# Kernel optimization log

Hardware: AMD Instinct MI355X
Metric: run time of the kernel (lower is better)

## Reference

```python
import jax, jax.numpy as jnp
import numpy as np

HEADS = 8
RANK = 4

def _lora(x, w_down, w_up, palette, in_dim, out_dim):
    # w_down: [RANK*in_dim, 15], w_up: [RANK*out_dim, 15], palette: [1, 15]
    down = (palette @ w_down.T).reshape(RANK, in_dim)   # [r, in]
    up = (palette @ w_up.T).reshape(out_dim, RANK)      # [out, r]
    return (x @ down.T) @ up.T                          # [..., out]


def setup_inputs() -> dict:
    key = jax.random.key(0)
    ks = jax.random.split(key, 16)
    B, S, D = 2, 2048, 1280
    def n(k, shape, std=0.02):
        return (jax.random.normal(k, shape, dtype=jnp.float32) * std).astype(jnp.float32)
    return {
        'hidden_states': jax.random.normal(ks[0], (B, S, D), dtype=jnp.float32),
        'color_palette': jax.random.uniform(ks[1], (1, 15), dtype=jnp.float32),
        'Wq': n(ks[2], (D, D)), 'Wk': n(ks[3], (D, D)),
        'Wv': n(ks[4], (D, D)), 'Wo': n(ks[5], (D, D)),
        'bo': jnp.zeros((D,), dtype=jnp.float32),
        'q_down': n(ks[6], (RANK * D, 15), 0.25), 'q_up': n(ks[7], (RANK * D, 15)),
        'k_down': n(ks[8], (RANK * D, 15), 0.25), 'k_up': n(ks[9], (RANK * D, 15)),
        'v_down': n(ks[10], (RANK * D, 15), 0.25), 'v_up': n(ks[11], (RANK * D, 15)),
        'o_down': n(ks[12], (RANK * D, 15), 0.25), 'o_up': n(ks[13], (RANK * D, 15)),
    }


def reference(hidden_states, color_palette, Wq, Wk, Wv, Wo, bo,
              q_down, q_up, k_down, k_up, v_down, v_up, o_down, o_up):
    B, S, D = hidden_states.shape
    H = HEADS
    hd = D // H
    scale = 1.0  # LoRA scale
    x = hidden_states
    # LoRA-augmented projections (self-attention: encoder_hidden_states = x)
    q = x @ Wq.T + scale * _lora(x, q_down, q_up, color_palette, D, D)
    k = x @ Wk.T + scale * _lora(x, k_down, k_up, color_palette, D, D)
    v = x @ Wv.T + scale * _lora(x, v_down, v_up, color_palette, D, D)
    # split heads: [B, S, D] -> [B, H, S, hd]
    q = q.reshape(B, S, H, hd).transpose(0, 2, 1, 3)
    k = k.reshape(B, S, H, hd).transpose(0, 2, 1, 3)
    v = v.reshape(B, S, H, hd).transpose(0, 2, 1, 3)
    attn_scale = 1.0 / jnp.sqrt(jnp.asarray(hd, dtype=q.dtype))
    scores = jnp.einsum('bhqd,bhkd->bhqk', q, k) * attn_scale
    probs = jax.nn.softmax(scores, axis=-1)
    out = jnp.einsum('bhqk,bhkd->bhqd', probs, v)
    out = out.transpose(0, 2, 1, 3).reshape(B, S, D)
    out = out @ Wo.T + bo + scale * _lora(out, o_down, o_up, color_palette, D, D)
    return out
```

## Files before the change

kernel.cpp:

```cpp
#include <hip/hip_runtime.h>

typedef unsigned short u16;
typedef unsigned int u32;
typedef __attribute__((ext_vector_type(4))) float floatx4;
typedef __attribute__((ext_vector_type(16))) float floatx16;
typedef __attribute__((ext_vector_type(8))) __bf16 bf16x8;
typedef __attribute__((ext_vector_type(2))) unsigned int u32x2;
typedef __attribute__((ext_vector_type(4))) unsigned int u32x4;

#define MFMA_BF16(a, b, c) __builtin_amdgcn_mfma_f32_16x16x32_bf16((a), (b), (c), 0, 0, 0)
#define MFMA32(a, b, c) __builtin_amdgcn_mfma_f32_32x32x16_bf16((a), (b), (c), 0, 0, 0)

typedef const __attribute__((address_space(1))) void* gas_ptr;
typedef __attribute__((address_space(3))) void* las_ptr;

__device__ __forceinline__ void gll16(const void* g, void* l) {
  __builtin_amdgcn_global_load_lds((gas_ptr)g, (las_ptr)l, 16, 0, 0);
}

__device__ __forceinline__ u16 f2bf(float x) {
  u32 u = __builtin_bit_cast(u32, x);
  u = (u + 0x7fffu + ((u >> 16) & 1u)) >> 16;
  return (u16)u;
}

__device__ __forceinline__ u32 cvtpk(float lo, float hi) {
  u32 r;
  asm("v_cvt_pk_bf16_f32 %0, %1, %2" : "=v"(r) : "v"(lo), "v"(hi));
  return r;
}

template <int WN>
__device__ __forceinline__ void vwait() {
  if constexpr (WN == 6) asm volatile("s_waitcnt vmcnt(6)" ::: "memory");
  else if constexpr (WN == 4) asm volatile("s_waitcnt vmcnt(4)" ::: "memory");
}

__global__ void prep_downup(const float* __restrict__ pal,
                            const float* __restrict__ qd, const float* __restrict__ qu,
                            const float* __restrict__ kd, const float* __restrict__ ku,
                            const float* __restrict__ vd, const float* __restrict__ vu,
                            const float* __restrict__ od, const float* __restrict__ ou,
                            float* __restrict__ down_f, float* __restrict__ up_f) {
  int tid = blockIdx.x * blockDim.x + threadIdx.x;
  int w = tid / 10240;
  int rem = tid - w * 10240;
  const float* dsrc = (w == 0) ? qd : (w == 1) ? kd : (w == 2) ? vd : od;
  const float* usrc = (w == 0) ? qu : (w == 1) ? ku : (w == 2) ? vu : ou;
  bool isdown = rem < 5120;
  int row = isdown ? rem : rem - 5120;
  const float* src = (isdown ? dsrc : usrc) + row * 15;
  float s = 0.f;
#pragma unroll
  for (int p = 0; p < 15; ++p) s += pal[p] * src[p];
  if (isdown) down_f[w * 5120 + row] = s;
  else        up_f[w * 5120 + row] = s;
}

__global__ void build_weff(const float* __restrict__ Wq, const float* __restrict__ Wk,
                           const float* __restrict__ Wv, const float* __restrict__ Wo,
                           const float* __restrict__ down_f, const float* __restrict__ up_f,
                           u16* __restrict__ weff_qkv, u16* __restrict__ weff_o) {
  int tid = blockIdx.x * blockDim.x + threadIdx.x;
  int w = tid / 1638400;
  int rem = tid - w * 1638400;
  int n = rem / 1280;
  int k = rem - n * 1280;
  const float* W = (w == 0) ? Wq : (w == 1) ? Wk : (w == 2) ? Wv : Wo;
  const float* up = up_f + w * 5120 + n * 4;
  const float* dn = down_f + w * 5120 + k;
  float v = W[rem] + up[0] * dn[0] + up[1] * dn[1280] + up[2] * dn[2560] + up[3] * dn[3840];
  u16 hv = f2bf(v);
  if (w < 3) weff_qkv[w * 1638400 + rem] = hv;
  else       weff_o[rem] = hv;
}

__global__ void cvt_x(const float4* __restrict__ x, ushort4* __restrict__ xb) {
  int i = blockIdx.x * blockDim.x + threadIdx.x;
  float4 v = x[i];
  ushort4 o;
  o.x = f2bf(v.x); o.y = f2bf(v.y); o.z = f2bf(v.z); o.w = f2bf(v.w);
  xb[i] = o;
}

__global__ __launch_bounds__(512) void gemm256_qkv(const u16* __restrict__ A, const u16* __restrict__ Bm,
                                                   u16* __restrict__ qb, u16* __restrict__ kb,
                                                   u16* __restrict__ vbuf, int K) {
  __shared__ __align__(16) u16 lA[2][16384];
  __shared__ __align__(16) u16 lB[2][16384];
  const int t = threadIdx.x;
  const int lane = t & 63;
  const int l15 = lane & 15, quad = lane >> 4;
  const int wid = t >> 6;
  const int wm = wid >> 2;
  const int wn = wid & 3;
  const int bm = blockIdx.x * 256;
  const int bn = blockIdx.y * 256;
  floatx4 acc[8][4] = {};

  const int r0 = t >> 3, pos = t & 7;
  const long sof0 = (long)r0 * K + ((pos + r0) & 7) * 8;
  const long sof1 = (long)(r0 + 64) * K + ((pos + r0 + 64) & 7) * 8;

  int afo[4][2], bfo[2][2];
#pragma unroll
  for (int ch = 0; ch < 2; ++ch) {
    int kc8 = ch * 4 + quad;
#pragma unroll
    for (int mi = 0; mi < 4; ++mi) {
      int ra = wm * 128 + mi * 16 + l15;
      afo[mi][ch] = ra * 64 + ((kc8 - ra) & 7) * 8;
    }
#pragma unroll
    for (int ni = 0; ni < 2; ++ni) {
      int rb = wn * 64 + ni * 16 + l15;
      bfo[ni][ch] = rb * 64 + ((kc8 - rb) & 7) * 8;
    }
  }

  const u16* Ab = A + (long)bm * K;
  const u16* Bb = Bm + (long)bn * K;

#define PHASE(CB, Q, SB, SMAT, SH, ST, WN)                                           \
  {                                                                                   \
    const u16* gsrc = (SMAT) ? Bb : Ab;                                               \
    u16* ld0 = ((SMAT) ? &lB[SB][0] : &lA[SB][0]) + ((SH) * 1024 + t) * 8;            \
    gll16(gsrc + sof0 + (long)(SH) * 128 * K + (long)(ST) * 64, ld0);                 \
    gll16(gsrc + sof1 + (long)(SH) * 128 * K + (long)(ST) * 64, ld0 + 4096);          \
    vwait<WN>();                                                                      \
    __builtin_amdgcn_s_barrier();                                                     \
    __builtin_amdgcn_sched_barrier(0);                                                \
    constexpr int mh = (Q) >> 1, nh = (Q) & 1;                                        \
    bf16x8 af[4][2], bfr[2][2];                                                       \
    _Pragma("unroll") for (int ch = 0; ch < 2; ++ch) {                                \
      _Pragma("unroll") for (int mi = 0; mi < 4; ++mi)                                \
        af[mi][ch] = *(const bf16x8*)(&lA[CB][0] + afo[mi][ch] + mh * 4096);          \
      _Pragma("unroll") for (int ni = 0; ni < 2; ++ni)                                \
        bfr[ni][ch] = *(const bf16x8*)(&lB[CB][0] + bfo[ni][ch] + nh * 2048);         \
    }                                                                                 \
    asm volatile("s_waitcnt lgkmcnt(0)" ::: "memory");                                \
    __builtin_amdgcn_sched_barrier(0);                                                \
    __builtin_amdgcn_s_setprio(1);                                                    \
    _Pragma("unroll") for (int ch = 0; ch < 2; ++ch)                                  \
      _Pragma("unroll") for (int mi = 0; mi < 4; ++mi)                                \
        _Pragma("unroll") for (int ni = 0; ni < 2; ++ni)                              \
          acc[mh * 4 + mi][nh * 2 + ni] =                                             \
              MFMA_BF16(af[mi][ch], bfr[ni][ch], acc[mh * 4 + mi][nh * 2 + ni]);      \
    __builtin_amdgcn_s_setprio(0);                                                    \
  }

  gll16(Ab + sof0, &lA[0][t * 8]);
  gll16(Ab + sof1, &lA[0][t * 8 + 4096]);
  gll16(Bb + sof0, &lB[0][t * 8]);
  gll16(Bb + sof1, &lB[0][t * 8 + 4096]);
  gll16(Ab + sof0 + 128L * K, &lA[0][(1024 + t) * 8]);
  gll16(Ab + sof1 + 128L * K, &lA[0][(1024 + t) * 8 + 4096]);
  gll16(Bb + sof0 + 128L * K, &lB[0][(1024 + t) * 8]);
  gll16(Bb + sof1 + 128L * K, &lB[0][(1024 + t) * 8 + 4096]);

  const int niter = K >> 7;
  for (int i = 0; i < niter; ++i) {
    const int t1 = 2 * i + 1, t2 = 2 * i + 2;
    PHASE(0, 0, 1, 0, 0, t1, 6);
    PHASE(0, 1, 1, 1, 0, t1, 4);
    PHASE(0, 2, 1, 0, 1, t1, 0);
    PHASE(0, 3, 1, 1, 1, t1, 0);
    PHASE(1, 0, 0, 0, 0, t2, 6);
    PHASE(1, 1, 0, 1, 0, t2, 4);
    PHASE(1, 2, 0, 0, 1, t2, 0);
    PHASE(1, 3, 0, 1, 1, t2, 0);
  }
#undef PHASE
  asm volatile("s_waitcnt vmcnt(0)" ::: "memory");

#pragma unroll
  for (int mi8 = 0; mi8 < 8; ++mi8) {
#pragma unroll
    for (int ni4 = 0; ni4 < 4; ++ni4) {
#pragma unroll
      for (int r = 0; r < 4; ++r) {
        int m = bm + wm * 128 + (mi8 >> 2) * 64 + (mi8 & 3) * 16 + quad * 4 + r;
        int n = bn + wn * 64 + (ni4 >> 1) * 32 + (ni4 & 1) * 16 + l15;
        u16 hv = f2bf(acc[mi8][ni4][r]);
        if (n < 1280) {
          qb[(long)m * 1280 + n] = hv;
        } else if (n < 2560) {
          kb[(long)m * 1280 + (n - 1280)] = hv;
        } else {
          vbuf[(long)m * 1280 + (n - 2560)] = hv;
        }
      }
    }
  }
}

__global__ __launch_bounds__(256) void vtrans(const u16* __restrict__ vbuf,
                                              u16* __restrict__ vtb) {
  __shared__ u16 tile[64 * 65];
  const int t = threadIdx.x;
  const int sb = blockIdx.x * 64, nb = blockIdx.y * 64, b = blockIdx.z;
  const u16* src = vbuf + ((long)(b * 2048 + sb)) * 1280 + nb;
#pragma unroll
  for (int it = 0; it < 16; ++it) {
    int idx = t + it * 256;
    int s = idx >> 6, n = idx & 63;
    tile[s * 65 + n] = src[(long)s * 1280 + n];
  }
  __syncthreads();
  u16* dst = vtb + ((long)(b * 1280 + nb)) * 2048 + sb;
#pragma unroll
  for (int it = 0; it < 16; ++it) {
    int idx = t + it * 256;
    int n = idx >> 6, s = idx & 63;
    dst[(long)n * 2048 + s] = tile[s * 65 + n];
  }
}

__global__ __launch_bounds__(256) void gemm128_o(const u16* __restrict__ A, const u16* __restrict__ Bm,
                                                 float* __restrict__ outf,
                                                 const float* __restrict__ bias, int K) {
  __shared__ __align__(16) u16 lA[128 * 64];
  __shared__ __align__(16) u16 lB[128 * 64];
  const int t = threadIdx.x;
  const int lane = t & 63;
  const int l15 = lane & 15, quad = lane >> 4;
  const int wid = t >> 6;
  const int wm = (wid >> 1) * 64;
  const int wn = (wid & 1) * 64;
  const int bm = blockIdx.x * 128;
  const int bn = blockIdx.y * 128;
  floatx4 acc[4][4] = {};

  int soff[4];
#pragma unroll
  for (int i = 0; i < 4; ++i) {
    int c = t + i * 256;
    int row = c >> 3, pos = c & 7;
    soff[i] = row * K + ((pos + row) & 7) * 8;
  }
  int afo[4][2], bfo[4][2];
#pragma unroll
  for (int i = 0; i < 4; ++i) {
#pragma unroll
    for (int ch = 0; ch < 2; ++ch) {
      int ra = wm + i * 16 + l15;
      int rb = wn + i * 16 + l15;
      int kc8 = ch * 4 + quad;
      afo[i][ch] = ra * 64 + ((kc8 - ra) & 7) * 8;
      bfo[i][ch] = rb * 64 + ((kc8 - rb) & 7) * 8;
    }
  }

  const u16* Ab = A + (long)bm * K;
  const u16* Bb = Bm + (long)bn * K;
  const int nkt = K >> 6;

  for (int kt = 0; kt < nkt; ++kt) {
    __syncthreads();
    const int k0 = kt * 64;
#pragma unroll
    for (int i = 0; i < 4; ++i) gll16(Ab + (long)soff[i] + k0, lA + (t + i * 256) * 8);
#pragma unroll
    for (int i = 0; i < 4; ++i) gll16(Bb + (long)soff[i] + k0, lB + (t + i * 256) * 8);
    __syncthreads();
#pragma unroll
    for (int ch = 0; ch < 2; ++ch) {
      bf16x8 af[4], bfr[4];
#pragma unroll
      for (int i = 0; i < 4; ++i) af[i] = *(const bf16x8*)(lA + afo[i][ch]);
#pragma unroll
      for (int i = 0; i < 4; ++i) bfr[i] = *(const bf16x8*)(lB + bfo[i][ch]);
#pragma unroll
      for (int i = 0; i < 4; ++i)
#pragma unroll
        for (int j = 0; j < 4; ++j)
          acc[i][j] = MFMA_BF16(af[i], bfr[j], acc[i][j]);
    }
  }

#pragma unroll
  for (int i = 0; i < 4; ++i) {
#pragma unroll
    for (int j = 0; j < 4; ++j) {
#pragma unroll
      for (int r = 0; r < 4; ++r) {
        int m = bm + wm + i * 16 + quad * 4 + r;
        int n = bn + wn + j * 16 + l15;
        outf[(long)m * 1280 + n] = acc[i][j][r] + bias[n];
      }
    }
  }
}

__global__ __launch_bounds__(512) void flash_attn(const u16* __restrict__ qb,
                                                  const u16* __restrict__ kb,
                                                  const u16* __restrict__ vtb,
                                                  u16* __restrict__ attn) {
  const int D = 1280, HD = 160;
  __shared__ __align__(16) u16 kv_lds[2][20480];
  const int t = threadIdx.x, lane = t & 63, wid = t >> 6;
  const int l31 = lane & 31, hi = lane >> 5;
  const int rg = wid >> 1, kh = wid & 1;
  const int bh = blockIdx.y, b = bh >> 3, h = bh & 7;
  const int q0 = blockIdx.x * 128 + rg * 32;
  const float kS = 0.11404582025f;

  bf16x8 aq[10];
  {
    const u16* qg = qb + ((long)(b * 2048 + q0 + l31)) * D + h * HD + hi * 8;
#pragma unroll
    for (int kw = 0; kw < 10; ++kw) aq[kw] = *(const bf16x8*)(qg + kw * 16);
  }

  const u16* sg[5];
  int sadv[5];
#pragma unroll
  for (int i = 0; i < 5; ++i) {
    int c = t + i * 512;
    if (c < 1280) {
      int key = c / 20, pos = c - key * 20;
      int ccol = pos - (key % 20);
      if (ccol < 0) ccol += 20;
      sg[i] = kb + ((long)(b * 2048 + key)) * D + h * HD + ccol * 8;
      sadv[i] = 64 * D;
    } else {
      int c2 = c - 1280;
      int vrow = c2 >> 3, swz = c2 & 7;
      int vcol = swz ^ (vrow & 7);
      sg[i] = vtb + ((long)(b * 1280 + h * HD + vrow)) * 2048 + vcol * 8;
      sadv[i] = 64;
    }
  }

  int kfo[10];
  {
    int key = kh * 32 + l31;
#pragma unroll
    for (int kw = 0; kw < 10; ++kw) {
      int g = kw * 2 + hi;
      int pos = (g + key) % 20;
      kfo[kw] = (key * 20 + pos) * 8;
    }
  }
  int vfo[5][2];
#pragma unroll
  for (int db = 0; db < 5; ++db) {
#pragma unroll
    for (int w = 0; w < 2; ++w) {
      int d = db * 32 + l31;
      int gc = kh * 4 + w * 2 + hi;
      int sw = gc ^ (d & 7);
      vfo[db][w] = 10240 + (d * 8 + sw) * 8;
    }
  }

  float l_sum = 0.f;
  floatx16 o_acc[5] = {};

#pragma unroll
  for (int i = 0; i < 5; ++i) {
    gll16(sg[i], &kv_lds[0][0] + (t + i * 512) * 8);
    sg[i] += sadv[i];
  }

  for (int kt0 = 0; kt0 < 32; ++kt0) {
    u16* cbase = &kv_lds[kt0 & 1][0];
    if (kt0 < 31) {
      u16* nbase = &kv_lds[(kt0 & 1) ^ 1][0];
#pragma unroll
      for (int i = 0; i < 5; ++i) {
        gll16(sg[i], nbase + (t + i * 512) * 8);
        sg[i] += sadv[i];
      }
      asm volatile("s_waitcnt vmcnt(5)" ::: "memory");
    } else {
      asm volatile("s_waitcnt vmcnt(0)" ::: "memory");
    }
    __builtin_amdgcn_s_barrier();
    __builtin_amdgcn_sched_barrier(0);

    floatx16 s = {};
    __builtin_amdgcn_s_setprio(1);
#pragma unroll
    for (int kw = 0; kw < 10; ++kw) {
      bf16x8 kf = *(const bf16x8*)(cbase + kfo[kw]);
      s = MFMA32(kf, aq[kw], s);
    }
    __builtin_amdgcn_s_setprio(0);

    float p[16];
#pragma unroll
    for (int r = 0; r < 16; ++r) {
      p[r] = __builtin_exp2f(fminf(s[r] * kS, 80.f));
      l_sum += p[r];
    }

    u32 c01 = cvtpk(p[0], p[1]),  c23 = cvtpk(p[2], p[3]);
    u32 c45 = cvtpk(p[4], p[5]),  c67 = cvtpk(p[6], p[7]);
    u32 c89 = cvtpk(p[8], p[9]),  cAB = cvtpk(p[10], p[11]);
    u32 cCD = cvtpk(p[12], p[13]), cEF = cvtpk(p[14], p[15]);

    u32x2 r02 = __builtin_amdgcn_permlane32_swap(c01, c45, false, false);
    u32x2 r13 = __builtin_amdgcn_permlane32_swap(c23, c67, false, false);
    u32x2 r46 = __builtin_amdgcn_permlane32_swap(c89, cCD, false, false);
    u32x2 r57 = __builtin_amdgcn_permlane32_swap(cAB, cEF, false, false);
    u32x4 pk0 = {r02[0], r13[0], r02[1], r13[1]};
    u32x4 pk1 = {r46[0], r57[0], r46[1], r57[1]};
    bf16x8 pa0 = __builtin_bit_cast(bf16x8, pk0);
    bf16x8 pa1 = __builtin_bit_cast(bf16x8, pk1);

    __builtin_amdgcn_s_setprio(1);
#pragma unroll
    for (int db = 0; db < 5; ++db) {
      bf16x8 v0 = *(const bf16x8*)(cbase + vfo[db][0]);
      bf16x8 v1 = *(const bf16x8*)(cbase + vfo[db][1]);
      o_acc[db] = MFMA32(pa0, v0, o_acc[db]);
      o_acc[db] = MFMA32(pa1, v1, o_acc[db]);
    }
    __builtin_amdgcn_s_setprio(0);
    __builtin_amdgcn_sched_barrier(0);
    __builtin_amdgcn_s_barrier();
  }

  float* lscr = (float*)&kv_lds[0][0];
  lscr[wid * 64 + lane] = l_sum;
  __syncthreads();
  float rl[16];
#pragma unroll
  for (int r = 0; r < 16; ++r) {
    int q32 = (r & 3) + 8 * (r >> 2) + 4 * hi;
    float tot = lscr[(rg * 2 + 0) * 64 + q32] + lscr[(rg * 2 + 0) * 64 + q32 + 32]
              + lscr[(rg * 2 + 1) * 64 + q32] + lscr[(rg * 2 + 1) * 64 + q32 + 32];
    rl[r] = 1.0f / tot;
  }
  __syncthreads();
  float* oscr = (float*)&kv_lds[0][0];
  if (kh == 1) {
#pragma unroll
    for (int db = 0; db < 5; ++db)
#pragma unroll
      for (int r = 0; r < 16; ++r)
        oscr[rg * 5120 + (db * 16 + r) * 64 + lane] = o_acc[db][r];
  }
  __syncthreads();
  if (kh == 0) {
#pragma unroll
    for (int db = 0; db < 5; ++db) {
#pragma unroll
      for (int r = 0; r < 16; ++r) {
        float v = (o_acc[db][r] + oscr[rg * 5120 + (db * 16 + r) * 64 + lane]) * rl[r];
        int row = q0 + (r & 3) + 8 * (r >> 2) + 4 * hi;
        int col = h * HD + db * 32 + l31;
        attn[((long)(b * 2048 + row)) * D + col] = f2bf(v);
      }
    }
  }
}

extern "C" void kernel_launch(void* const* d_in, const int* in_sizes, int n_in,
                              void* d_out, int out_size, void* d_ws, size_t ws_size,
                              hipStream_t stream) {
  const float* x   = (const float*)d_in[0];
  const float* pal = (const float*)d_in[1];
  const float* Wq  = (const float*)d_in[2];
  const float* Wk  = (const float*)d_in[3];
  const float* Wv  = (const float*)d_in[4];
  const float* Wo  = (const float*)d_in[5];
  const float* bo  = (const float*)d_in[6];
  const float* qd  = (const float*)d_in[7];
  const float* qu  = (const float*)d_in[8];
  const float* kd  = (const float*)d_in[9];
  const float* ku  = (const float*)d_in[10];
  const float* vd  = (const float*)d_in[11];
  const float* vu  = (const float*)d_in[12];
  const float* od  = (const float*)d_in[13];
  const float* ou  = (const float*)d_in[14];
  float* out = (float*)d_out;

  char* ws = (char*)d_ws;
  u16* xb       = (u16*)(ws);
  u16* weff_qkv = (u16*)(ws + 10485760);
  u16* weff_o   = (u16*)(ws + 20316160);
  u16* qbuf     = (u16*)(ws + 23592960);
  u16* kbuf     = (u16*)(ws + 34078720);
  u16* vtb      = (u16*)(ws + 44564480);
  u16* attn     = (u16*)(ws + 55050240);
  float* down_f = (float*)(ws + 65536000);
  float* up_f   = (float*)(ws + 65617920);
  u16* vbuf     = (u16*)(ws + 65699840);

  prep_downup<<<160, 256, 0, stream>>>(pal, qd, qu, kd, ku, vd, vu, od, ou, down_f, up_f);
  build_weff<<<25600, 256, 0, stream>>>(Wq, Wk, Wv, Wo, down_f, up_f, weff_qkv, weff_o);
  cvt_x<<<5120, 256, 0, stream>>>((const float4*)x, (ushort4*)xb);
  gemm256_qkv<<<dim3(16, 15), 512, 0, stream>>>(xb, weff_qkv, qbuf, kbuf, vbuf, 1280);
  vtrans<<<dim3(32, 20, 2), 256, 0, stream>>>(vbuf, vtb);
  flash_attn<<<dim3(16, 16), 512, 0, stream>>>(qbuf, kbuf, vtb, attn);
  gemm128_o<<<dim3(32, 10), 256, 0, stream>>>(attn, weff_o, out, bo, 1280);
}
```

Before: 268.7 us.

## Software-pipeline PV matmul behind next QK and swizzle block order for cache locality

The flash attention loop is restructured so the PV MFMAs for the previous tile run after the current tile's QK MFMAs, with K and V loads staggered across the two LDS buffers so their lifetimes overlap. QK accumulation is split into two independent accumulators to shorten the MFMA dependency chain. The K LDS swizzle now uses 3*key mod 20 to reduce bank conflicts, and both the QKV GEMM and attention grids are remapped with an XCD-aware swizzle for L2 locality. The cost is more live registers and more complex buffer indexing that could hurt occupancy or correctness.

```diff
diff --git a/kernel.cpp b/kernel.cpp
--- a/kernel.cpp
+++ b/kernel.cpp
@@ -94,8 +94,10 @@
   const int wid = t >> 6;
   const int wm = wid >> 2;
   const int wn = wid & 3;
-  const int bm = blockIdx.x * 256;
-  const int bn = blockIdx.y * 256;
+  const int l = blockIdx.y * 16 + blockIdx.x;
+  const int v = (l & 7) * 30 + (l >> 3);
+  const int bm = (v & 15) * 256;
+  const int bn = (v >> 4) * 256;
   floatx4 acc[8][4] = {};
 
   const int r0 = t >> 3, pos = t & 7;
@@ -301,8 +303,11 @@
   const int t = threadIdx.x, lane = t & 63, wid = t >> 6;
   const int l31 = lane & 31, hi = lane >> 5;
   const int rg = wid >> 1, kh = wid & 1;
-  const int bh = blockIdx.y, b = bh >> 3, h = bh & 7;
-  const int q0 = blockIdx.x * 128 + rg * 32;
+  const int lflat = blockIdx.y * 16 + blockIdx.x;
+  const int vswz = (lflat & 7) * 32 + (lflat >> 3);
+  const int qi = vswz & 15, bh = vswz >> 4;
+  const int b = bh >> 3, h = bh & 7;
+  const int q0 = qi * 128 + rg * 32;
   const float kS = 0.11404582025f;
 
   bf16x8 aq[10];
@@ -319,9 +324,9 @@
     int c = t + i * 512;
     if (c < 1280) {
       int key = c / 20, pos = c - key * 20;
-      int ccol = pos - (key % 20);
-      if (ccol < 0) ccol += 20;
-      sg[i] = kb + ((long)(b * 2048 + key)) * D + h * HD + ccol * 8;
+      int g = pos - (3 * key) % 20;
+      if (g < 0) g += 20;
+      sg[i] = kb + ((long)(b * 2048 + key)) * D + h * HD + g * 8;
       sadv[i] = 64 * D;
     } else {
       int c2 = c - 1280;
@@ -335,10 +340,12 @@
   int kfo[10];
   {
     int key = kh * 32 + l31;
+    int r3 = (3 * key) % 20;
 #pragma unroll
     for (int kw = 0; kw < 10; ++kw) {
       int g = kw * 2 + hi;
-      int pos = (g + key) % 20;
+      int pos = g + r3;
+      if (pos >= 20) pos -= 20;
       kfo[kw] = (key * 20 + pos) * 8;
     }
   }
@@ -356,71 +363,85 @@
 
   float l_sum = 0.f;
   floatx16 o_acc[5] = {};
-
-#pragma unroll
-  for (int i = 0; i < 5; ++i) {
-    gll16(sg[i], &kv_lds[0][0] + (t + i * 512) * 8);
-    sg[i] += sadv[i];
-  }
+  bf16x8 paA = {}, paB = {};
+
+  gll16(sg[0], &kv_lds[0][t * 8]);           sg[0] += sadv[0];
+  gll16(sg[1], &kv_lds[0][(t + 512) * 8]);   sg[1] += sadv[1];
+  if (wid < 4) { gll16(sg[2], &kv_lds[0][(t + 1024) * 8]); sg[2] += sadv[2]; }
 
   for (int kt0 = 0; kt0 < 32; ++kt0) {
-    u16* cbase = &kv_lds[kt0 & 1][0];
+    u16* kd = &kv_lds[(kt0 + 1) & 1][0];
+    u16* vd = &kv_lds[kt0 & 1][0];
     if (kt0 < 31) {
-      u16* nbase = &kv_lds[(kt0 & 1) ^ 1][0];
-#pragma unroll
-      for (int i = 0; i < 5; ++i) {
-        gll16(sg[i], nbase + (t + i * 512) * 8);
-        sg[i] += sadv[i];
-      }
-      asm volatile("s_waitcnt vmcnt(5)" ::: "memory");
-    } else {
-      asm volatile("s_waitcnt vmcnt(0)" ::: "memory");
-    }
+      gll16(sg[0], kd + t * 8);          sg[0] += sadv[0];
+      gll16(sg[1], kd + (t + 512) * 8);  sg[1] += sadv[1];
+      if (wid < 4) { gll16(sg[2], kd + (t + 1024) * 8); sg[2] += sadv[2]; }
+    }
+    if (wid >= 4) { gll16(sg[2], vd + (t + 1024) * 8); sg[2] += sadv[2]; }
+    gll16(sg[3], vd + (t + 1536) * 8);  sg[3] += sadv[3];
+    gll16(sg[4], vd + (t + 2048) * 8);  sg[4] += sadv[4];
+
+    if (kt0 < 31) asm volatile("s_waitcnt vmcnt(5)" ::: "memory");
+    else          asm volatile("s_waitcnt vmcnt(0)" ::: "memory");
     __builtin_amdgcn_s_barrier();
     __builtin_amdgcn_sched_barrier(0);
 
-    floatx16 s = {};
-    __builtin_amdgcn_s_setprio(1);
-#pragma unroll
-    for (int kw = 0; kw < 10; ++kw) {
-      bf16x8 kf = *(const bf16x8*)(cbase + kfo[kw]);
-      s = MFMA32(kf, aq[kw], s);
-    }
-    __builtin_amdgcn_s_setprio(0);
+    const u16* kbase = &kv_lds[kt0 & 1][0];
+    const u16* vbase = &kv_lds[(kt0 + 1) & 1][0];
+
+    floatx16 s0 = {}, s1 = {};
+#pragma unroll
+    for (int kw = 0; kw < 5; ++kw) {
+      bf16x8 k0 = *(const bf16x8*)(kbase + kfo[kw * 2]);
+      bf16x8 k1 = *(const bf16x8*)(kbase + kfo[kw * 2 + 1]);
+      s0 = MFMA32(k0, aq[kw * 2], s0);
+      s1 = MFMA32(k1, aq[kw * 2 + 1], s1);
+    }
+
+    if (kt0 > 0) {
+#pragma unroll
+      for (int db = 0; db < 5; ++db) {
+        bf16x8 v0 = *(const bf16x8*)(vbase + vfo[db][0]);
+        bf16x8 v1 = *(const bf16x8*)(vbase + vfo[db][1]);
+        o_acc[db] = MFMA32(paA, v0, o_acc[db]);
+        o_acc[db] = MFMA32(paB, v1, o_acc[db]);
+      }
+    }
 
     float p[16];
 #pragma unroll
     for (int r = 0; r < 16; ++r) {
-      p[r] = __builtin_exp2f(fminf(s[r] * kS, 80.f));
+      p[r] = __builtin_exp2f(fminf((s0[r] + s1[r]) * kS, 80.f));
       l_sum += p[r];
     }
-
     u32 c01 = cvtpk(p[0], p[1]),  c23 = cvtpk(p[2], p[3]);
     u32 c45 = cvtpk(p[4], p[5]),  c67 = cvtpk(p[6], p[7]);
     u32 c89 = cvtpk(p[8], p[9]),  cAB = cvtpk(p[10], p[11]);
     u32 cCD = cvtpk(p[12], p[13]), cEF = cvtpk(p[14], p[15]);
-
     u32x2 r02 = __builtin_amdgcn_permlane32_swap(c01, c45, false, false);
     u32x2 r13 = __builtin_amdgcn_permlane32_swap(c23, c67, false, false);
     u32x2 r46 = __builtin_amdgcn_permlane32_swap(c89, cCD, false, false);
     u32x2 r57 = __builtin_amdgcn_permlane32_swap(cAB, cEF, false, false);
     u32x4 pk0 = {r02[0], r13[0], r02[1], r13[1]};
     u32x4 pk1 = {r46[0], r57[0], r46[1], r57[1]};
-    bf16x8 pa0 = __builtin_bit_cast(bf16x8, pk0);
-    bf16x8 pa1 = __builtin_bit_cast(bf16x8, pk1);
-
-    __builtin_amdgcn_s_setprio(1);
-#pragma unroll
-    for (int db = 0; db < 5; ++db) {
-      bf16x8 v0 = *(const bf16x8*)(cbase + vfo[db][0]);
-      bf16x8 v1 = *(const bf16x8*)(cbase + vfo[db][1]);
-      o_acc[db] = MFMA32(pa0, v0, o_acc[db]);
-      o_acc[db] = MFMA32(pa1, v1, o_acc[db]);
-    }
-    __builtin_amdgcn_s_setprio(0);
+    paA = __builtin_bit_cast(bf16x8, pk0);
+    paB = __builtin_bit_cast(bf16x8, pk1);
+
     __builtin_amdgcn_sched_barrier(0);
     __builtin_amdgcn_s_barrier();
   }
+
+  {
+    const u16* vbase = &kv_lds[1][0];
+#pragma unroll
+    for (int db = 0; db < 5; ++db) {
+      bf16x8 v0 = *(const bf16x8*)(vbase + vfo[db][0]);
+      bf16x8 v1 = *(const bf16x8*)(vbase + vfo[db][1]);
+      o_acc[db] = MFMA32(paA, v0, o_acc[db]);
+      o_acc[db] = MFMA32(paB, v1, o_acc[db]);
+    }
+  }
+  __syncthreads();
 
   float* lscr = (float*)&kv_lds[0][0];
   lscr[wid * 64 + lane] = l_sum;
```

Result: no change. 267.5 us (-0.5%).
